# Optimization experiments

Measured on AMD Instinct MI355X. Metric: run time of the kernel, lower is better.

## Reference

```python
import jax, jax.numpy as jnp
import numpy as np

FP8 = jnp.float8_e4m3fn

def setup_inputs() -> dict:
    key = jax.random.key(0)
    k_in, k_w = jax.random.split(key)
    M, H = 16384, 4096
    input = jax.random.normal(k_in, (M, H), dtype=jnp.float32)
    # learned fp8 weight, materialized as float32 then quantized in reference
    weight = jax.random.normal(k_w, (H, H), dtype=jnp.float32) * 0.02
    scale_b = jnp.ones((1, H), dtype=jnp.float32)  # per-column dequant scale
    return {"input": input, "weight": weight, "scale_b": scale_b, "world_size": 8}

def reference(input, weight, scale_b, world_size):
    # fp8 quantize input and weight (torch._scaled_mm consumes fp8 operands)
    a = input.astype(FP8).astype(jnp.float32)            # [M, H]
    b = weight.astype(FP8).astype(jnp.float32)           # [H, H]
    scale_a = jnp.ones((input.shape[0], 1), dtype=jnp.float32)  # [M, 1]
    # scaled_mm: (a @ b) * scale_a * scale_b, out_dtype=fp16
    out = (a @ b) * scale_a * scale_b                    # [M, H] fp32 accumulate
    out = out.astype(jnp.float16)
    # reduce_scatter along dim 0: sum corresponding shards across world_size ranks
    M, H = out.shape
    rs = out.reshape(world_size, M // world_size, H).sum(axis=0)  # [M/world, H]
    return rs.astype(jnp.float16)
```

## Files before the change

### kernel.cpp

```cpp
#include <hip/hip_runtime.h>

#define MFULL 16384
#define MOUT  2048
#define H     4096
#define WS    8
#define BK    64
#define BM    128
#define BN    256
#define NT    (H / BK)

typedef _Float16 f16x8 __attribute__((ext_vector_type(8)));
typedef _Float16 f16x4 __attribute__((ext_vector_type(4)));
typedef _Float16 f16x2 __attribute__((ext_vector_type(2)));
typedef float    f32x4 __attribute__((ext_vector_type(4)));
typedef float    f32x2 __attribute__((ext_vector_type(2)));

__device__ __forceinline__ void fp8_rt4(float4& v) {
    int p0 = __builtin_amdgcn_cvt_pk_fp8_f32(v.x, v.y, 0, false);
    int p1 = __builtin_amdgcn_cvt_pk_fp8_f32(v.z, v.w, 0, false);
    f32x2 r0 = __builtin_amdgcn_cvt_pk_f32_fp8(p0, false);
    f32x2 r1 = __builtin_amdgcn_cvt_pk_f32_fp8(p1, false);
    v.x = r0.x; v.y = r0.y; v.z = r1.x; v.w = r1.y;
}

__device__ __forceinline__ void async_copy16(const void* g, void* l) {
    __builtin_amdgcn_global_load_lds(
        (const __attribute__((address_space(1))) void*)g,
        (__attribute__((address_space(3))) void*)l, 16, 0, 0);
}

__global__ void reduce_quant_a(const float* __restrict__ in,
                               _Float16* __restrict__ aq) {
    int idx = blockIdx.x * 256 + threadIdx.x;
    int r = idx >> 10;
    int k = (idx & 1023) * 4;
    const float* p = in + (size_t)r * H + k;
    float4 acc = {0.f, 0.f, 0.f, 0.f};
#pragma unroll
    for (int s = 0; s < WS; ++s) {
        float4 v = *(const float4*)(p + (size_t)s * MOUT * H);
        fp8_rt4(v);
        acc.x += v.x; acc.y += v.y; acc.z += v.z; acc.w += v.w;
    }
    f16x4 h = { (_Float16)acc.x, (_Float16)acc.y, (_Float16)acc.z, (_Float16)acc.w };
    *(f16x4*)(aq + (size_t)r * H + k) = h;
}

__global__ void quant_transpose_b(const float* __restrict__ w,
                                  _Float16* __restrict__ bt) {
    __shared__ _Float16 tile[64][66];
    int t  = threadIdx.x;
    int n0 = blockIdx.x * 64;
    int k0 = blockIdx.y * 64;
#pragma unroll
    for (int i = 0; i < 4; ++i) {
        int lin = i * 256 + t;
        int kl = lin >> 4;
        int nl = (lin & 15) * 4;
        float4 v = *(const float4*)(w + (size_t)(k0 + kl) * H + n0 + nl);
        fp8_rt4(v);
        tile[kl][nl + 0] = (_Float16)v.x;
        tile[kl][nl + 1] = (_Float16)v.y;
        tile[kl][nl + 2] = (_Float16)v.z;
        tile[kl][nl + 3] = (_Float16)v.w;
    }
    __syncthreads();
#pragma unroll
    for (int i = 0; i < 8; ++i) {
        int lin = i * 256 + t;
        int kl = (lin & 31) * 2;
        int nl = lin >> 5;
        f16x2 hv = { tile[kl][nl], tile[kl + 1][nl] };
        *(f16x2*)(bt + (size_t)(n0 + nl) * H + k0 + kl) = hv;
    }
}

__global__ __launch_bounds__(512, 2) void gemm_rs(
    const _Float16* __restrict__ A, const _Float16* __restrict__ Bt,
    const float* __restrict__ scale_b, float* __restrict__ out) {
    __shared__ _Float16 As[3][BM * BK];
    __shared__ _Float16 Bs[3][BN * BK];

    const int tid  = threadIdx.x;
    const int wid  = tid >> 6;
    const int lane = tid & 63;
    const int quad = lane >> 4;
    const int l16  = lane & 15;
    const int bm   = blockIdx.y * BM;
    const int bn   = blockIdx.x * BN;
    const int wm   = (wid >> 2) * 64;
    const int wn   = (wid & 3) * 64;

    f32x4 acc[4][4] = {};

    const _Float16* Ab = A  + (size_t)bm * H;
    const _Float16* Bb = Bt + (size_t)bn * H;

    size_t gaA[2]; int laA[2];
    size_t gaB[4]; int laB[4];
#pragma unroll
    for (int u = 0; u < 2; ++u) {
        int c = u * 512 + tid;
        int row = c >> 3, slot = c & 7;
        int kc = slot ^ ((row >> 1) & 7);
        gaA[u] = (size_t)row * H + kc * 8;
        laA[u] = c * 16;
    }
#pragma unroll
    for (int u = 0; u < 4; ++u) {
        int c = u * 512 + tid;
        int row = c >> 3, slot = c & 7;
        int kc = slot ^ ((row >> 1) & 7);
        gaB[u] = (size_t)row * H + kc * 8;
        laB[u] = c * 16;
    }

    int aOff[4][2], bOff[4][2];
#pragma unroll
    for (int i = 0; i < 4; ++i) {
        int rowA = wm + i * 16 + l16;
        int rowB = wn + i * 16 + l16;
#pragma unroll
        for (int h = 0; h < 2; ++h) {
            int sA = (h * 4 + quad) ^ ((rowA >> 1) & 7);
            int sB = (h * 4 + quad) ^ ((rowB >> 1) & 7);
            aOff[i][h] = rowA * BK + sA * 8;
            bOff[i][h] = rowB * BK + sB * 8;
        }
    }

#define STAGE(bufi, koff)                                                   \
    {                                                                       \
        char* aL = (char*)&As[bufi][0];                                     \
        char* bL = (char*)&Bs[bufi][0];                                     \
        _Pragma("unroll")                                                   \
        for (int u = 0; u < 2; ++u)                                         \
            async_copy16(Ab + gaA[u] + (koff), aL + laA[u]);                \
        _Pragma("unroll")                                                   \
        for (int u = 0; u < 4; ++u)                                         \
            async_copy16(Bb + gaB[u] + (koff), bL + laB[u]);                \
    }

#define COMPUTE(bufi)                                                       \
    {                                                                       \
        const _Float16* aP = &As[bufi][0];                                  \
        const _Float16* bP = &Bs[bufi][0];                                  \
        f16x8 af[4][2], bf[4][2];                                           \
        _Pragma("unroll")                                                   \
        for (int i = 0; i < 4; ++i) {                                       \
            _Pragma("unroll")                                               \
            for (int h = 0; h < 2; ++h) {                                   \
                af[i][h] = *(const f16x8*)(aP + aOff[i][h]);                \
                bf[i][h] = *(const f16x8*)(bP + bOff[i][h]);                \
            }                                                               \
        }                                                                   \
        __builtin_amdgcn_s_setprio(1);                                      \
        _Pragma("unroll")                                                   \
        for (int h = 0; h < 2; ++h)                                         \
            _Pragma("unroll")                                               \
            for (int i = 0; i < 4; ++i)                                     \
                _Pragma("unroll")                                           \
                for (int j = 0; j < 4; ++j)                                 \
                    acc[i][j] = __builtin_amdgcn_mfma_f32_16x16x32_f16(     \
                        af[i][h], bf[j][h], acc[i][j], 0, 0, 0);            \
        __builtin_amdgcn_s_setprio(0);                                      \
    }

    STAGE(0, 0);
    STAGE(1, BK);
    asm volatile("s_waitcnt vmcnt(6)" ::: "memory");
    __builtin_amdgcn_s_barrier();
    asm volatile("" ::: "memory");

    int cur = 0;
    for (int t = 0; t < NT - 2; ++t) {
        int b2 = cur + 2; if (b2 >= 3) b2 -= 3;
        STAGE(b2, (t + 2) * BK);
        COMPUTE(cur);
        asm volatile("s_waitcnt vmcnt(6)" ::: "memory");
        __builtin_amdgcn_s_barrier();
        asm volatile("" ::: "memory");
        cur = cur + 1; if (cur >= 3) cur = 0;
    }
    COMPUTE(cur);
    asm volatile("s_waitcnt vmcnt(0)" ::: "memory");
    __builtin_amdgcn_s_barrier();
    asm volatile("" ::: "memory");
    cur = cur + 1; if (cur >= 3) cur = 0;
    COMPUTE(cur);

#undef STAGE
#undef COMPUTE

#pragma unroll
    for (int j = 0; j < 4; ++j) {
        int col = bn + wn + j * 16 + l16;
        float sb = scale_b[col];
#pragma unroll
        for (int i = 0; i < 4; ++i) {
#pragma unroll
            for (int r = 0; r < 4; ++r) {
                int row = bm + wm + i * 16 + quad * 4 + r;
                float v = acc[i][j][r] * sb;
                out[(size_t)row * H + col] = (float)(_Float16)v;
            }
        }
    }
}

extern "C" void kernel_launch(void* const* d_in, const int* in_sizes, int n_in,
                              void* d_out, int out_size, void* d_ws, size_t ws_size,
                              hipStream_t stream) {
    const float* input   = (const float*)d_in[0];
    const float* weight  = (const float*)d_in[1];
    const float* scale_b = (const float*)d_in[2];
    float* out = (float*)d_out;

    _Float16* aq = (_Float16*)d_ws;
    _Float16* bt = aq + (size_t)MOUT * H;

    reduce_quant_a<<<(MOUT * H / 4) / 256, 256, 0, stream>>>(input, aq);
    quant_transpose_b<<<dim3(H / 64, H / 64), 256, 0, stream>>>(weight, bt);
    gemm_rs<<<dim3(H / BN, MOUT / BM), 512, 0, stream>>>(aq, bt, scale_b, out);
}
```

Baseline: 514.3 us.

## Interleave LDS reads, async global loads and MFMA groups in ping-pong phases

Result: faster. 498.8 us (-3.0%).

```diff
diff --git a/kernel.cpp b/kernel.cpp
--- a/kernel.cpp
+++ b/kernel.cpp
@@ -129,29 +129,38 @@
         }
     }
 
-#define STAGE(bufi, koff)                                                   \
+#define FENCE asm volatile("" ::: "memory")
+#define BAR   __builtin_amdgcn_s_barrier()
+
+#define MG(afv, bfv, j)                                                     \
+    _Pragma("unroll")                                                       \
+    for (int i = 0; i < 4; ++i)                                             \
+        acc[i][j] = __builtin_amdgcn_mfma_f32_16x16x32_f16(                 \
+            afv[i], bfv, acc[i][j], 0, 0, 0);
+
+#define STAGE_ALL(bufi, koff)                                               \
     {                                                                       \
-        char* aL = (char*)&As[bufi][0];                                     \
-        char* bL = (char*)&Bs[bufi][0];                                     \
+        char* aL_ = (char*)&As[bufi][0];                                    \
+        char* bL_ = (char*)&Bs[bufi][0];                                    \
         _Pragma("unroll")                                                   \
         for (int u = 0; u < 2; ++u)                                         \
-            async_copy16(Ab + gaA[u] + (koff), aL + laA[u]);                \
+            async_copy16(Ab + gaA[u] + (koff), aL_ + laA[u]);               \
         _Pragma("unroll")                                                   \
         for (int u = 0; u < 4; ++u)                                         \
-            async_copy16(Bb + gaB[u] + (koff), bL + laB[u]);                \
-    }
-
-#define COMPUTE(bufi)                                                       \
+            async_copy16(Bb + gaB[u] + (koff), bL_ + laB[u]);               \
+    }
+
+#define COMPUTE_MONO(bufi)                                                  \
     {                                                                       \
-        const _Float16* aP = &As[bufi][0];                                  \
-        const _Float16* bP = &Bs[bufi][0];                                  \
+        const _Float16* aP_ = &As[bufi][0];                                 \
+        const _Float16* bP_ = &Bs[bufi][0];                                 \
         f16x8 af[4][2], bf[4][2];                                           \
         _Pragma("unroll")                                                   \
         for (int i = 0; i < 4; ++i) {                                       \
             _Pragma("unroll")                                               \
             for (int h = 0; h < 2; ++h) {                                   \
-                af[i][h] = *(const f16x8*)(aP + aOff[i][h]);                \
-                bf[i][h] = *(const f16x8*)(bP + bOff[i][h]);                \
+                af[i][h] = *(const f16x8*)(aP_ + aOff[i][h]);               \
+                bf[i][h] = *(const f16x8*)(bP_ + bOff[i][h]);               \
             }                                                               \
         }                                                                   \
         __builtin_amdgcn_s_setprio(1);                                      \
@@ -166,31 +175,85 @@
         __builtin_amdgcn_s_setprio(0);                                      \
     }
 
-    STAGE(0, 0);
-    STAGE(1, BK);
+    STAGE_ALL(0, 0);
+    STAGE_ALL(1, BK);
     asm volatile("s_waitcnt vmcnt(6)" ::: "memory");
-    __builtin_amdgcn_s_barrier();
-    asm volatile("" ::: "memory");
+    BAR;
+    FENCE;
 
     int cur = 0;
     for (int t = 0; t < NT - 2; ++t) {
         int b2 = cur + 2; if (b2 >= 3) b2 -= 3;
-        STAGE(b2, (t + 2) * BK);
-        COMPUTE(cur);
+        const _Float16* aP = &As[cur][0];
+        const _Float16* bP = &Bs[cur][0];
+        char* aL = (char*)&As[b2][0];
+        char* bL = (char*)&Bs[b2][0];
+        const size_t ko2 = (size_t)(t + 2) * BK;
+
+        f16x8 af0[4], af1[4];
+
+#pragma unroll
+        for (int i = 0; i < 4; ++i) af0[i] = *(const f16x8*)(aP + aOff[i][0]);
+        f16x8 b00 = *(const f16x8*)(bP + bOff[0][0]);
+        f16x8 b10 = *(const f16x8*)(bP + bOff[1][0]);
+#pragma unroll
+        for (int u = 0; u < 2; ++u) async_copy16(Ab + gaA[u] + ko2, aL + laA[u]);
+        FENCE; BAR;
+        __builtin_amdgcn_s_setprio(1);
+        MG(af0, b00, 0);
+        MG(af0, b10, 1);
+        __builtin_amdgcn_s_setprio(0);
+        FENCE; BAR;
+
+        f16x8 b20 = *(const f16x8*)(bP + bOff[2][0]);
+        f16x8 b30 = *(const f16x8*)(bP + bOff[3][0]);
+#pragma unroll
+        for (int u = 0; u < 2; ++u) async_copy16(Bb + gaB[u] + ko2, bL + laB[u]);
+        FENCE; BAR;
+        __builtin_amdgcn_s_setprio(1);
+        MG(af0, b20, 2);
+        MG(af0, b30, 3);
+        __builtin_amdgcn_s_setprio(0);
+        FENCE; BAR;
+
+#pragma unroll
+        for (int i = 0; i < 4; ++i) af1[i] = *(const f16x8*)(aP + aOff[i][1]);
+        f16x8 b01 = *(const f16x8*)(bP + bOff[0][1]);
+        f16x8 b11 = *(const f16x8*)(bP + bOff[1][1]);
+#pragma unroll
+        for (int u = 2; u < 4; ++u) async_copy16(Bb + gaB[u] + ko2, bL + laB[u]);
+        FENCE; BAR;
+        __builtin_amdgcn_s_setprio(1);
+        MG(af1, b01, 0);
+        MG(af1, b11, 1);
+        __builtin_amdgcn_s_setprio(0);
+        FENCE; BAR;
+
+        f16x8 b21 = *(const f16x8*)(bP + bOff[2][1]);
+        f16x8 b31 = *(const f16x8*)(bP + bOff[3][1]);
         asm volatile("s_waitcnt vmcnt(6)" ::: "memory");
-        __builtin_amdgcn_s_barrier();
-        asm volatile("" ::: "memory");
+        FENCE; BAR;
+        __builtin_amdgcn_s_setprio(1);
+        MG(af1, b21, 2);
+        MG(af1, b31, 3);
+        __builtin_amdgcn_s_setprio(0);
+        FENCE; BAR;
+
         cur = cur + 1; if (cur >= 3) cur = 0;
     }
-    COMPUTE(cur);
+
+    COMPUTE_MONO(cur);
     asm volatile("s_waitcnt vmcnt(0)" ::: "memory");
-    __builtin_amdgcn_s_barrier();
-    asm volatile("" ::: "memory");
+    BAR;
+    FENCE;
     cur = cur + 1; if (cur >= 3) cur = 0;
-    COMPUTE(cur);
-
-#undef STAGE
-#undef COMPUTE
+    COMPUTE_MONO(cur);
+
+#undef FENCE
+#undef BAR
+#undef MG
+#undef STAGE_ALL
+#undef COMPUTE_MONO
 
 #pragma unroll
     for (int j = 0; j < 4; ++j) {
```
